# Kernel tuning notes

Hardware: AMD Instinct MI355X
Metric: run time of the kernel (lower is better)

## Reference

```python
import jax, jax.numpy as jnp
import numpy as np

B, NINP, NHID = 8192, 256, 1024
NB_IN, NB_OUT = 1, 8
BS_OUT = NHID // NB_OUT          # 128
ATT_OUT = BS_OUT * 4             # 512
TOPKVAL = 4


@jax.custom_vjp
def blocked_grad(x, mask):
    # forward is identity; backward masks the gradient (RIMs blocked_grad)
    return x

def _bg_fwd(x, mask):
    return x, mask

def _bg_bwd(mask, g):
    return (g * mask, jnp.zeros_like(mask))

blocked_grad.defvjp(_bg_fwd, _bg_bwd)


def setup_inputs() -> dict:
    key = jax.random.key(0)
    ks = jax.random.split(key, 12)
    p = lambda i, shape, s: s * jax.random.normal(ks[i], shape, dtype=jnp.float32)
    return {
        "inp": jax.random.normal(ks[0], (B, NB_IN * NINP), dtype=jnp.float32),
        "hx": jax.random.normal(ks[1], (B, NHID), dtype=jnp.float32),
        "step": 0,
        "Wq1": p(2, (NB_OUT, BS_OUT, 64), 0.01),
        "Wk1": p(3, (2, NINP, 64), 0.01),
        "Wv1": p(4, (2, NINP, ATT_OUT), 0.01),
        "Wq2": p(5, (NB_OUT, BS_OUT, 64), 0.01),
        "Wk2": p(6, (NB_OUT, BS_OUT, 64), 0.01),
        "Wv2": p(7, (NB_OUT, BS_OUT, 64), 0.01),
        "fc_w": p(8, (64, BS_OUT), 0.05),
        "fc_b": jnp.zeros((BS_OUT,), jnp.float32),
        "gate_w": p(9, (64, BS_OUT), 0.05),
        "gate_b": jnp.zeros((BS_OUT,), jnp.float32),
        "gru_wi": p(10, (NB_OUT, ATT_OUT, 3 * BS_OUT), 0.05),
        "gru_wh": p(11, (NB_OUT, BS_OUT, 3 * BS_OUT), 0.05),
        "gru_bi": jnp.zeros((NB_OUT, 3 * BS_OUT), jnp.float32),
        "gru_bh": jnp.zeros((NB_OUT, 3 * BS_OUT), jnp.float32),
    }


def _block_gru(x, h, wi, wh, bi, bh):
    # x: [B, K, ATT_OUT], h: [B, K, BS_OUT]; blockified GRUCell == per-block GRU
    gx = jnp.einsum('bkd,kde->bke', x, wi) + bi
    gh = jnp.einsum('bkd,kde->bke', h, wh) + bh
    xr, xz, xn = jnp.split(gx, 3, axis=-1)
    hr, hz, hn = jnp.split(gh, 3, axis=-1)
    r = jax.nn.sigmoid(xr + hr)
    z = jax.nn.sigmoid(xz + hz)
    n = jnp.tanh(xn + r * hn)
    return (1.0 - z) * n + z * h


def reference(inp, hx, step, Wq1, Wk1, Wv1, Wq2, Wk2, Wv2,
              fc_w, fc_b, gate_w, gate_b, gru_wi, gru_wh, gru_bi, gru_bh):
    b = inp.shape[0]
    x = inp.reshape(b, NB_IN, NINP)                              # repeat factor (num_modules_read_input-1)=1
    kv = jnp.concatenate([jnp.zeros_like(x[:, :1]), x], axis=1)  # [b, 2, NINP] (null slot first)
    hq = hx.reshape(b, NB_OUT, BS_OUT)

    # input attention (n_head=1, d_k=64, skip_write -> identity fc, no residual gating)
    q = jnp.einsum('bkd,kde->bke', hq, Wq1)                      # [b, 8, 64]
    kk = jnp.einsum('bmd,mde->bme', kv, Wk1)                     # [b, 2, 64]
    vv = jnp.einsum('bmd,mde->bme', kv, Wv1)                     # [b, 2, 512]
    iatt = jax.nn.softmax(jnp.einsum('bke,bme->bkm', q, kk) / 8.0, axis=-1)  # temp=sqrt(64)
    inp_use = jnp.einsum('bkm,bme->bke', iatt, vv)               # [b, 8, 512]

    # top-k block selection: zero out blocks most attentive to the null slot
    null_score = iatt[:, :, 0]
    _, bottom_idx = jax.lax.top_k(null_score, NB_OUT - TOPKVAL)
    mask = jnp.ones((b, NB_OUT), inp.dtype)
    mask = mask.at[jnp.arange(b)[:, None], bottom_idx].set(0.0)
    mask = jax.lax.stop_gradient(mask)

    hx_new = _block_gru(inp_use, hq, gru_wi, gru_wh, gru_bi, gru_bh)  # [b, 8, 128]

    # communication attention (n_head=4, d_k=d_v=16, gated residual form)
    g = blocked_grad(hx_new, mask[:, :, None])
    q2 = jnp.einsum('bkd,kde->bke', g, Wq2).reshape(b, NB_OUT, 4, 16)
    k2 = jnp.einsum('bkd,kde->bke', g, Wk2).reshape(b, NB_OUT, 4, 16)
    v2 = jnp.einsum('bkd,kde->bke', g, Wv2).reshape(b, NB_OUT, 4, 16)
    attn2 = jax.nn.softmax(jnp.einsum('bqhd,bkhd->bhqk', q2, k2) / 4.0, axis=-1)  # temp=sqrt(16)
    o = jnp.einsum('bhqk,bkhd->bqhd', attn2, v2).reshape(b, NB_OUT, 64)
    att = jax.nn.sigmoid(o @ gate_w + gate_b) * jnp.tanh(o @ fc_w + fc_b)  # [b, 8, 128]
    hx_new = hx_new + att

    mask_full = jnp.repeat(mask[:, :, None], BS_OUT, axis=2).reshape(b, NHID)
    hx_out = mask_full * hx_new.reshape(b, NHID) + (1.0 - mask_full) * hx
    return hx_out, mask_full
```

## Files before the change

kernel.cpp:

```cpp
#include <hip/hip_runtime.h>
#include <cstdint>
#include <cstddef>

#define NB 8192

typedef __attribute__((ext_vector_type(4))) float f32x4;
typedef __attribute__((ext_vector_type(8))) short bf16x8;

__device__ __forceinline__ float sigmoidf_(float x){ return 1.0f/(1.0f+expf(-x)); }

__device__ __forceinline__ unsigned short f2bf(float f){
    union { float f; unsigned u; } v; v.f = f;
    unsigned u = v.u;
    return (unsigned short)((u + 0x7fffu + ((u >> 16) & 1u)) >> 16);
}
__device__ __forceinline__ float bf2f(unsigned short b){
    union { unsigned u; float f; } v; v.u = ((unsigned)b) << 16;
    return v.f;
}
__device__ __forceinline__ void ld8f(const unsigned short* p, float* f){
    uint4 u = *(const uint4*)p;
    f[0]=bf2f(u.x&0xffff); f[1]=bf2f(u.x>>16);
    f[2]=bf2f(u.y&0xffff); f[3]=bf2f(u.y>>16);
    f[4]=bf2f(u.z&0xffff); f[5]=bf2f(u.z>>16);
    f[6]=bf2f(u.w&0xffff); f[7]=bf2f(u.w>>16);
}

__global__ __launch_bounds__(256) void gemm_nn(
    const float* __restrict__ A, int lda, int aZ,
    const float* __restrict__ W, int wZ, int ldw,
    float* __restrict__ C, int ldc, int cZ,
    int K)
{
    __shared__ float As[16][68];
    __shared__ float Ws[16][64];
    const int tid = threadIdx.x;
    const int tx = tid & 15, ty = tid >> 4;
    const int rowBase = blockIdx.y * 64;
    const int colBase = blockIdx.x * 64;
    A += (size_t)blockIdx.z * aZ;
    W += (size_t)blockIdx.z * wZ;
    C += (size_t)blockIdx.z * cZ;

    float acc[4][4] = {};
    for (int k0 = 0; k0 < K; k0 += 16) {
#pragma unroll
        for (int i = 0; i < 4; ++i) {
            int e = i * 256 + tid;
            int m = e >> 4, kk = e & 15;
            As[kk][m] = A[(size_t)(rowBase + m) * lda + (k0 + kk)];
        }
#pragma unroll
        for (int i = 0; i < 4; ++i) {
            int e = i * 256 + tid;
            int kk = e >> 6, n = e & 63;
            Ws[kk][n] = W[(size_t)(k0 + kk) * ldw + (colBase + n)];
        }
        __syncthreads();
#pragma unroll
        for (int kk = 0; kk < 16; ++kk) {
            const float4 a4 = *(const float4*)&As[kk][ty * 4];
            const float4 b4 = *(const float4*)&Ws[kk][tx * 4];
            const float a[4] = {a4.x, a4.y, a4.z, a4.w};
            const float b[4] = {b4.x, b4.y, b4.z, b4.w};
#pragma unroll
            for (int i = 0; i < 4; ++i)
#pragma unroll
                for (int j = 0; j < 4; ++j)
                    acc[i][j] = fmaf(a[i], b[j], acc[i][j]);
        }
        __syncthreads();
    }
#pragma unroll
    for (int i = 0; i < 4; ++i) {
        float* Cr = C + (size_t)(rowBase + ty * 4 + i) * ldc + colBase + tx * 4;
#pragma unroll
        for (int j = 0; j < 4; ++j) Cr[j] = acc[i][j];
    }
}

__global__ __launch_bounds__(256) void score_mask_k(
    const float* __restrict__ qbuf,
    const float* __restrict__ kk1,
    float* __restrict__ cbuf,
    float* __restrict__ maskb)
{
    const int b = blockIdx.x * 256 + threadIdx.x;
    const float* kr = kk1 + (size_t)b * 64;
    double s[8];
#pragma unroll
    for (int k = 0; k < 8; ++k) {
        const float* qr = qbuf + (size_t)b * 512 + k * 64;
        double acc = 0.0;
#pragma unroll
        for (int d = 0; d < 64; ++d) acc = fma((double)qr[d], (double)kr[d], acc);
        s[k] = acc / 8.0;
    }
#pragma unroll
    for (int k = 0; k < 8; ++k) {
        int rank = 0;
#pragma unroll
        for (int j = 0; j < 8; ++j)
            rank += (s[j] < s[k]) || (s[j] == s[k] && j < k);
        maskb[(size_t)b * 8 + k] = (rank < 4) ? 0.f : 1.f;
        cbuf[(size_t)b * 8 + k] = (float)(1.0 / (1.0 + exp(-s[k])));
    }
}

__global__ __launch_bounds__(256) void cast_bf(
    const float* __restrict__ inp, const float* __restrict__ hx,
    unsigned short* __restrict__ inp_bf, unsigned short* __restrict__ hx_bf)
{
    const int idx = blockIdx.x * 256 + threadIdx.x;
    const int NI = 524288;
    const float* src; unsigned short* dst; int i;
    if (idx < NI) { src = inp; dst = inp_bf; i = idx; }
    else          { src = hx;  dst = hx_bf;  i = idx - NI; }
    float4 v = *(const float4*)(src + (size_t)i * 4);
    uint2 u;
    u.x = (unsigned)f2bf(v.x) | ((unsigned)f2bf(v.y) << 16);
    u.y = (unsigned)f2bf(v.z) | ((unsigned)f2bf(v.w) << 16);
    *(uint2*)(dst + (size_t)i * 4) = u;
}

__global__ __launch_bounds__(256) void prep_w(
    const float* __restrict__ gwi, const float* __restrict__ gwh,
    const float* __restrict__ Wq2, const float* __restrict__ Wk2, const float* __restrict__ Wv2,
    const float* __restrict__ gate_w, const float* __restrict__ fc_w,
    unsigned short* __restrict__ wi_t,
    unsigned short* __restrict__ wh_t,
    unsigned short* __restrict__ w2_t,
    unsigned short* __restrict__ gfc_t)
{
    int idx = blockIdx.x * 256 + threadIdx.x;
    const int N1 = 8*384*512, N2 = 8*384*128, N3 = 8*192*128, N4 = 2*128*64;
    if (idx < N1) {
        int k = idx / 196608, r = idx % 196608, j = r / 512, e = r % 512;
        wi_t[idx] = f2bf(gwi[((size_t)k*512 + e)*384 + j]); return;
    }
    idx -= N1;
    if (idx < N2) {
        int k = idx / 49152, r = idx % 49152, j = r / 128, d = r % 128;
        wh_t[idx] = f2bf(gwh[((size_t)k*128 + d)*384 + j]); return;
    }
    idx -= N2;
    if (idx < N3) {
        int k = idx / 24576, r = idx % 24576, n = r / 128, d = r % 128;
        const float* Wsrc = (n < 64) ? Wq2 : ((n < 128) ? Wk2 : Wv2);
        w2_t[idx] = f2bf(Wsrc[((size_t)k*128 + d)*64 + (n & 63)]); return;
    }
    idx -= N3;
    if (idx < N4) {
        int g = idx / 8192, r = idx % 8192, j = r / 64, d = r % 64;
        gfc_t[idx] = f2bf((g ? fc_w : gate_w)[d*128 + j]);
    }
}

template<int ASRC_F32, int EPI>
__global__ __launch_bounds__(256) void gemm_bf(
    const void* __restrict__ Av, int lda, int aZ,
    const unsigned short* __restrict__ Bt, int bZ, int ldb,
    unsigned short* __restrict__ C, int ldc, long cZ,
    int K)
{
    __shared__ unsigned short As[64][72];
    __shared__ unsigned short Bs[64][72];
    const int tid = threadIdx.x;
    const int wave = tid >> 6, lane = tid & 63;
    const int wr = wave >> 1, wc = wave & 1;
    const int lr = lane & 15, lo = lane >> 4;
    const int rowBase = blockIdx.y * 64, colBase = blockIdx.x * 64;
    const int z = blockIdx.z;

    const f32x4 zero = {0.f, 0.f, 0.f, 0.f};
    f32x4 acc[2][2];
    acc[0][0]=zero; acc[0][1]=zero; acc[1][0]=zero; acc[1][1]=zero;

    const unsigned short* B = Bt + (size_t)z * bZ;
    for (int k0 = 0; k0 < K; k0 += 64) {
        if (ASRC_F32) {
            const float* A = (const float*)Av + (size_t)z * aZ;
#pragma unroll
            for (int i = 0; i < 4; ++i) {
                int c = i*256 + tid;
                int r = c >> 4, kc = (c & 15) << 2;
                float4 a4 = *(const float4*)(A + (size_t)(rowBase + r) * lda + k0 + kc);
                unsigned short* p = &As[r][kc];
                p[0]=f2bf(a4.x); p[1]=f2bf(a4.y); p[2]=f2bf(a4.z); p[3]=f2bf(a4.w);
            }
        } else {
            const unsigned short* A = (const unsigned short*)Av + (size_t)z * aZ;
#pragma unroll
            for (int i = 0; i < 2; ++i) {
                int c = i*256 + tid;
                int r = c >> 3, kc = (c & 7) << 3;
                *(uint4*)&As[r][kc] = *(const uint4*)(A + (size_t)(rowBase + r) * lda + k0 + kc);
            }
        }
#pragma unroll
        for (int i = 0; i < 2; ++i) {
            int c = i*256 + tid;
            int n = c >> 3, kc = (c & 7) << 3;
            *(uint4*)&Bs[n][kc] = *(const uint4*)(B + (size_t)(colBase + n) * ldb + k0 + kc);
        }
        __syncthreads();
#pragma unroll
        for (int ks = 0; ks < 64; ks += 32) {
            bf16x8 a0 = *(const bf16x8*)&As[wr*32 + lr][ks + lo*8];
            bf16x8 a1 = *(const bf16x8*)&As[wr*32 + 16 + lr][ks + lo*8];
            bf16x8 b0 = *(const bf16x8*)&Bs[wc*32 + lr][ks + lo*8];
            bf16x8 b1 = *(const bf16x8*)&Bs[wc*32 + 16 + lr][ks + lo*8];
            acc[0][0] = __builtin_amdgcn_mfma_f32_16x16x32_bf16(a0,b0,acc[0][0],0,0,0);
            acc[0][1] = __builtin_amdgcn_mfma_f32_16x16x32_bf16(a0,b1,acc[0][1],0,0,0);
            acc[1][0] = __builtin_amdgcn_mfma_f32_16x16x32_bf16(a1,b0,acc[1][0],0,0,0);
            acc[1][1] = __builtin_amdgcn_mfma_f32_16x16x32_bf16(a1,b1,acc[1][1],0,0,0);
        }
        __syncthreads();
    }
#pragma unroll
    for (int i = 0; i < 2; ++i)
#pragma unroll
    for (int j = 0; j < 2; ++j)
#pragma unroll
    for (int r = 0; r < 4; ++r) {
        int row = rowBase + wr*32 + i*16 + lo*4 + r;
        int col = colBase + wc*32 + j*16 + lr;
        float v = acc[i][j][r];
        if (EPI == 0) C[(size_t)row * ldc + (size_t)z * cZ + col] = f2bf(v);
        else          C[(size_t)z * cZ + (size_t)col * ldc + row] = f2bf(v);
    }
}

__global__ __launch_bounds__(256) void gemm_gxh(
    const unsigned short* __restrict__ inp_bf,
    const unsigned short* __restrict__ wc_t,
    const unsigned short* __restrict__ hx_bf,
    const unsigned short* __restrict__ wh_t,
    const float* __restrict__ cbuf,
    const float* __restrict__ gbi, const float* __restrict__ gbh,
    unsigned short* __restrict__ comb)
{
    __shared__ unsigned short As[64][72];
    __shared__ unsigned short Bs[128][72];
    const int tid = threadIdx.x;
    const int wave = tid >> 6, lane = tid & 63;
    const int wr = wave >> 1, wc = wave & 1;
    const int lr = lane & 15, lo = lane >> 4;
    const int rowBase = blockIdx.y * 64, colBase = blockIdx.x * 128;
    const int z = blockIdx.z;

    const f32x4 zero = {0.f, 0.f, 0.f, 0.f};
    f32x4 acc1[2][2][2], acc2[2][2][2];
#pragma unroll
    for (int t = 0; t < 2; ++t)
#pragma unroll
    for (int i = 0; i < 2; ++i)
#pragma unroll
    for (int j = 0; j < 2; ++j) { acc1[t][i][j] = zero; acc2[t][i][j] = zero; }

    const unsigned short* B1 = wc_t + (size_t)z * (384*256);
    for (int k0 = 0; k0 < 256; k0 += 64) {
#pragma unroll
        for (int i = 0; i < 2; ++i) {
            int c = i*256 + tid;
            int r = c >> 3, kc = (c & 7) << 3;
            *(uint4*)&As[r][kc] = *(const uint4*)(inp_bf + (size_t)(rowBase + r) * 256 + k0 + kc);
        }
#pragma unroll
        for (int i = 0; i < 4; ++i) {
            int c = i*256 + tid;
            int n = c >> 3, kc = (c & 7) << 3;
            *(uint4*)&Bs[n][kc] = *(const uint4*)(B1 + (size_t)(colBase + n) * 256 + k0 + kc);
        }
        __syncthreads();
#pragma unroll
        for (int ks = 0; ks < 64; ks += 32) {
            bf16x8 a0 = *(const bf16x8*)&As[wr*32 + lr][ks + lo*8];
            bf16x8 a1 = *(const bf16x8*)&As[wr*32 + 16 + lr][ks + lo*8];
#pragma unroll
            for (int t = 0; t < 2; ++t) {
                bf16x8 b0 = *(const bf16x8*)&Bs[t*64 + wc*32 + lr][ks + lo*8];
                bf16x8 b1 = *(const bf16x8*)&Bs[t*64 + wc*32 + 16 + lr][ks + lo*8];
                acc1[t][0][0] = __builtin_amdgcn_mfma_f32_16x16x32_bf16(a0,b0,acc1[t][0][0],0,0,0);
                acc1[t][0][1] = __builtin_amdgcn_mfma_f32_16x16x32_bf16(a0,b1,acc1[t][0][1],0,0,0);
                acc1[t][1][0] = __builtin_amdgcn_mfma_f32_16x16x32_bf16(a1,b0,acc1[t][1][0],0,0,0);
                acc1[t][1][1] = __builtin_amdgcn_mfma_f32_16x16x32_bf16(a1,b1,acc1[t][1][1],0,0,0);
            }
        }
        __syncthreads();
    }
    const unsigned short* B2 = wh_t + (size_t)z * (384*128);
    for (int k0 = 0; k0 < 128; k0 += 64) {
#pragma unroll
        for (int i = 0; i < 2; ++i) {
            int c = i*256 + tid;
            int r = c >> 3, kc = (c & 7) << 3;
            *(uint4*)&As[r][kc] = *(const uint4*)(hx_bf + (size_t)(rowBase + r) * 1024 + z*128 + k0 + kc);
        }
#pragma unroll
        for (int i = 0; i < 4; ++i) {
            int c = i*256 + tid;
            int n = c >> 3, kc = (c & 7) << 3;
            *(uint4*)&Bs[n][kc] = *(const uint4*)(B2 + (size_t)(colBase + n) * 128 + k0 + kc);
        }
        __syncthreads();
#pragma unroll
        for (int ks = 0; ks < 64; ks += 32) {
            bf16x8 a0 = *(const bf16x8*)&As[wr*32 + lr][ks + lo*8];
            bf16x8 a1 = *(const bf16x8*)&As[wr*32 + 16 + lr][ks + lo*8];
#pragma unroll
            for (int t = 0; t < 2; ++t) {
                bf16x8 b0 = *(const bf16x8*)&Bs[t*64 + wc*32 + lr][ks + lo*8];
                bf16x8 b1 = *(const bf16x8*)&Bs[t*64 + wc*32 + 16 + lr][ks + lo*8];
                acc2[t][0][0] = __builtin_amdgcn_mfma_f32_16x16x32_bf16(a0,b0,acc2[t][0][0],0,0,0);
                acc2[t][0][1] = __builtin_amdgcn_mfma_f32_16x16x32_bf16(a0,b1,acc2[t][0][1],0,0,0);
                acc2[t][1][0] = __builtin_amdgcn_mfma_f32_16x16x32_bf16(a1,b0,acc2[t][1][0],0,0,0);
                acc2[t][1][1] = __builtin_amdgcn_mfma_f32_16x16x32_bf16(a1,b1,acc2[t][1][1],0,0,0);
            }
        }
        __syncthreads();
    }
#pragma unroll
    for (int t = 0; t < 2; ++t)
#pragma unroll
    for (int i = 0; i < 2; ++i)
#pragma unroll
    for (int j = 0; j < 2; ++j)
#pragma unroll
    for (int r = 0; r < 4; ++r) {
        int row = rowBase + wr*32 + i*16 + lo*4 + r;
        int col = colBase + t*64 + wc*32 + j*16 + lr;
        float c = cbuf[(size_t)row * 8 + z];
        float v1 = fmaf(c, acc1[t][i][j][r], gbi[z*384 + col]);
        float v2 = acc2[t][i][j][r] + gbh[z*384 + col];
        size_t base = ((size_t)z * 8192 + row) * 512;
        if (col < 256) comb[base + col] = f2bf(v1 + v2);
        else { comb[base + col] = f2bf(v1); comb[base + col + 128] = f2bf(v2); }
    }
}

__global__ __launch_bounds__(256) void gru_all(
    const unsigned short* __restrict__ comb, const float* __restrict__ hx,
    unsigned short* __restrict__ hxn)
{
    const int idx = blockIdx.x * 256 + threadIdx.x;
    const int j = idx & 127, k = (idx >> 7) & 7, b = idx >> 10;
    const size_t base = ((size_t)k * 8192 + b) * 512;
    const float rz = bf2f(comb[base + j]);
    const float zz = bf2f(comb[base + 128 + j]);
    const float xn = bf2f(comb[base + 256 + j]);
    const float hn = bf2f(comb[base + 384 + j]);
    const float r = sigmoidf_(rz), z = sigmoidf_(zz);
    const float n = tanhf(fmaf(r, hn, xn));
    const float h = hx[idx];
    hxn[idx] = f2bf((1.f - z) * n + z * h);
}

__global__ __launch_bounds__(256) void attn2_bf(
    const unsigned short* __restrict__ qkv, unsigned short* __restrict__ o)
{
    const int idx = blockIdx.x * 256 + threadIdx.x;
    const int qb = idx & 7, h = (idx >> 3) & 3, b = idx >> 5;
    const unsigned short* rowb = qkv + (size_t)b * 1536;
    float qv[16];
    ld8f(rowb + qb*192 + h*16, qv); ld8f(rowb + qb*192 + h*16 + 8, qv + 8);
    float sc[8]; float mx = -1e30f;
#pragma unroll
    for (int kb = 0; kb < 8; ++kb) {
        float kv[16];
        ld8f(rowb + kb*192 + 64 + h*16, kv); ld8f(rowb + kb*192 + 64 + h*16 + 8, kv + 8);
        float a = 0.f;
#pragma unroll
        for (int d = 0; d < 16; ++d) a = fmaf(qv[d], kv[d], a);
        sc[kb] = a * 0.25f;
        mx = fmaxf(mx, sc[kb]);
    }
    float sum = 0.f;
#pragma unroll
    for (int kb = 0; kb < 8; ++kb) { sc[kb] = expf(sc[kb] - mx); sum += sc[kb]; }
    const float inv = 1.f / sum;
    float oa[16];
#pragma unroll
    for (int d = 0; d < 16; ++d) oa[d] = 0.f;
#pragma unroll
    for (int kb = 0; kb < 8; ++kb) {
        float vv[16];
        ld8f(rowb + kb*192 + 128 + h*16, vv); ld8f(rowb + kb*192 + 128 + h*16 + 8, vv + 8);
#pragma unroll
        for (int d = 0; d < 16; ++d) oa[d] = fmaf(sc[kb], vv[d], oa[d]);
    }
    unsigned short t[16];
#pragma unroll
    for (int d = 0; d < 16; ++d) t[d] = f2bf(oa[d] * inv);
    uint4 u0, u1;
    u0.x = (unsigned)t[0] | ((unsigned)t[1]<<16);  u0.y = (unsigned)t[2] | ((unsigned)t[3]<<16);
    u0.z = (unsigned)t[4] | ((unsigned)t[5]<<16);  u0.w = (unsigned)t[6] | ((unsigned)t[7]<<16);
    u1.x = (unsigned)t[8] | ((unsigned)t[9]<<16);  u1.y = (unsigned)t[10]| ((unsigned)t[11]<<16);
    u1.z = (unsigned)t[12]| ((unsigned)t[13]<<16); u1.w = (unsigned)t[14]| ((unsigned)t[15]<<16);
    unsigned short* op = o + (size_t)(b*8 + qb) * 64 + h*16;
    *(uint4*)op = u0; *(uint4*)(op + 8) = u1;
}

__global__ __launch_bounds__(256) void gatefc_final(
    const unsigned short* __restrict__ o,
    const unsigned short* __restrict__ gfc_t,
    const float* __restrict__ gate_b, const float* __restrict__ fc_b,
    const unsigned short* __restrict__ hxn,
    const float* __restrict__ hx,
    const float* __restrict__ maskb,
    float* __restrict__ out)
{
    __shared__ unsigned short As[64][72];
    __shared__ unsigned short Bg[64][72];
    __shared__ unsigned short Bf[64][72];
    const int tid = threadIdx.x;
    const int wave = tid >> 6, lane = tid & 63;
    const int wr = wave >> 1, wc = wave & 1;
    const int lr = lane & 15, lo = lane >> 4;
    const int rowBase = blockIdx.y * 64, colBase = blockIdx.x * 64;

#pragma unroll
    for (int i = 0; i < 2; ++i) {
        int c = i*256 + tid;
        int r = c >> 3, kc = (c & 7) << 3;
        *(uint4*)&As[r][kc] = *(const uint4*)(o + (size_t)(rowBase + r) * 64 + kc);
        *(uint4*)&Bg[r][kc] = *(const uint4*)(gfc_t + (size_t)(colBase + r) * 64 + kc);
        *(uint4*)&Bf[r][kc] = *(const uint4*)(gfc_t + 8192 + (size_t)(colBase + r) * 64 + kc);
    }
    __syncthreads();

    const f32x4 zero = {0.f, 0.f, 0.f, 0.f};
    f32x4 ag[2][2], af[2][2];
    ag[0][0]=zero; ag[0][1]=zero; ag[1][0]=zero; ag[1][1]=zero;
    af[0][0]=zero; af[0][1]=zero; af[1][0]=zero; af[1][1]=zero;
#pragma unroll
    for (int ks = 0; ks < 64; ks += 32) {
        bf16x8 a0 = *(const bf16x8*)&As[wr*32 + lr][ks + lo*8];
        bf16x8 a1 = *(const bf16x8*)&As[wr*32 + 16 + lr][ks + lo*8];
        bf16x8 g0 = *(const bf16x8*)&Bg[wc*32 + lr][ks + lo*8];
        bf16x8 g1 = *(const bf16x8*)&Bg[wc*32 + 16 + lr][ks + lo*8];
        bf16x8 f0 = *(const bf16x8*)&Bf[wc*32 + lr][ks + lo*8];
        bf16x8 f1 = *(const bf16x8*)&Bf[wc*32 + 16 + lr][ks + lo*8];
        ag[0][0] = __builtin_amdgcn_mfma_f32_16x16x32_bf16(a0,g0,ag[0][0],0,0,0);
        ag[0][1] = __builtin_amdgcn_mfma_f32_16x16x32_bf16(a0,g1,ag[0][1],0,0,0);
        ag[1][0] = __builtin_amdgcn_mfma_f32_16x16x32_bf16(a1,g0,ag[1][0],0,0,0);
        ag[1][1] = __builtin_amdgcn_mfma_f32_16x16x32_bf16(a1,g1,ag[1][1],0,0,0);
        af[0][0] = __builtin_amdgcn_mfma_f32_16x16x32_bf16(a0,f0,af[0][0],0,0,0);
        af[0][1] = __builtin_amdgcn_mfma_f32_16x16x32_bf16(a0,f1,af[0][1],0,0,0);
        af[1][0] = __builtin_amdgcn_mfma_f32_16x16x32_bf16(a1,f0,af[1][0],0,0,0);
        af[1][1] = __builtin_amdgcn_mfma_f32_16x16x32_bf16(a1,f1,af[1][1],0,0,0);
    }
#pragma unroll
    for (int i = 0; i < 2; ++i)
#pragma unroll
    for (int j = 0; j < 2; ++j)
#pragma unroll
    for (int r = 0; r < 4; ++r) {
        int m   = rowBase + wr*32 + i*16 + lo*4 + r;
        int col = colBase + wc*32 + j*16 + lr;
        float g = sigmoidf_(ag[i][j][r] + gate_b[col]);
        float f = tanhf(af[i][j][r] + fc_b[col]);
        float att = g * f;
        size_t oidx = (size_t)m * 128 + col;
        float msk = maskb[m];
        float hnv = bf2f(hxn[oidx]) + att;
        out[oidx] = msk * hnv + (1.f - msk) * hx[oidx];
        out[(size_t)NB * 1024 + oidx] = msk;
    }
}

extern "C" void kernel_launch(void* const* d_in, const int* in_sizes, int n_in,
                              void* d_out, int out_size, void* d_ws, size_t ws_size,
                              hipStream_t stream)
{
    (void)in_sizes; (void)n_in; (void)out_size; (void)ws_size;
    const float* inp    = (const float*)d_in[0];
    const float* hx     = (const float*)d_in[1];
    const float* Wq1    = (const float*)d_in[3];
    const float* Wk1    = (const float*)d_in[4];
    const float* Wv1    = (const float*)d_in[5];
    const float* Wq2    = (const float*)d_in[6];
    const float* Wk2    = (const float*)d_in[7];
    const float* Wv2    = (const float*)d_in[8];
    const float* fc_w   = (const float*)d_in[9];
    const float* fc_b   = (const float*)d_in[10];
    const float* gate_w = (const float*)d_in[11];
    const float* gate_b = (const float*)d_in[12];
    const float* gwi    = (const float*)d_in[13];
    const float* gwh    = (const float*)d_in[14];
    const float* gbi    = (const float*)d_in[15];
    const float* gbh    = (const float*)d_in[16];
    float* out = (float*)d_out;

    char* W = (char*)d_ws;
    float* cbuf  = (float*)(W + 0x0);
    float* maskb = (float*)(W + 0x40000);
    float* kk1f  = (float*)(W + 0x80000);
    float* qbuff = (float*)(W + 0x280000);
    unsigned short* inp_bf = (unsigned short*)(W + 0x1280000);
    unsigned short* hx_bf  = (unsigned short*)(W + 0x1680000);
    unsigned short* wi_t   = (unsigned short*)(W + 0x2680000);
    unsigned short* wh_t   = (unsigned short*)(W + 0x2980000);
    unsigned short* w2_t   = (unsigned short*)(W + 0x2A40000);
    unsigned short* gfc_t  = (unsigned short*)(W + 0x2AA0000);
    unsigned short* wc_t   = (unsigned short*)(W + 0x2AA8000);
    unsigned short* comb   = (unsigned short*)(W + 0x2C28000);
    unsigned short* hxn    = (unsigned short*)(W + 0x6C28000);
    unsigned short* qkv    = comb;
    unsigned short* o_bf   = (unsigned short*)(W + 0x2C28000 + 25165824);

    const dim3 blk(256);

    gemm_nn<<<dim3(1, 128, 1), blk, 0, stream>>>(inp, 256, 0, Wk1 + 256*64, 0, 64, kk1f, 64, 0, 256);
    gemm_nn<<<dim3(1, 128, 8), blk, 0, stream>>>(hx, 1024, 128, Wq1, 128*64, 64, qbuff, 512, 64, 128);
    score_mask_k<<<dim3(32), blk, 0, stream>>>(qbuff, kk1f, cbuf, maskb);

    cast_bf<<<dim3(10240), blk, 0, stream>>>(inp, hx, inp_bf, hx_bf);
    prep_w<<<dim3(8512), blk, 0, stream>>>(gwi, gwh, Wq2, Wk2, Wv2, gate_w, fc_w,
                                           wi_t, wh_t, w2_t, gfc_t);

    gemm_bf<1, 1><<<dim3(6, 4, 8), blk, 0, stream>>>(
        Wv1 + 256*512, 512, 0, wi_t, 384*512, 512, wc_t, 256, (long)384*256, 512);

    gemm_gxh<<<dim3(3, 128, 8), blk, 0, stream>>>(inp_bf, wc_t, hx_bf, wh_t, cbuf, gbi, gbh, comb);

    gru_all<<<dim3(32768), blk, 0, stream>>>(comb, hx, hxn);

    gemm_bf<0, 0><<<dim3(3, 128, 8), blk, 0, stream>>>(
        hxn, 1024, 128, w2_t, 192*128, 128, qkv, 1536, 192L, 128);

    attn2_bf<<<dim3(1024), blk, 0, stream>>>(qkv, o_bf);

    gatefc_final<<<dim3(2, 1024), blk, 0, stream>>>(o_bf, gfc_t, gate_b, fc_b,
                                                    hxn, hx, maskb, out);
}
```

Baseline: 372.8 us.

## Fuse GRU gate epilogue into gate GEMM and move score GEMMs to split-bf16 MFMA

The GRU elementwise pass is folded into the gate GEMM epilogue. Weight columns are repacked so each block holds matching r/z/n column groups, which removes the large intermediate comb buffer and its separate kernel. The fp32 FMA score GEMMs become a single MFMA kernel that uses hi/lo bf16 splitting (four MFMAs per tile) to keep near-fp32 accuracy for the top-k mask. The cast and weight-prep kernels are merged into one, and the Wv1×gwi combine reads the fp32 weights directly. The cost is more MFMA work and register pressure in the fused kernel, plus a small risk that the split-bf16 scores flip mask decisions relative to fp64.

```diff
diff --git a/kernel.cpp b/kernel.cpp
--- a/kernel.cpp
+++ b/kernel.cpp
@@ -25,65 +25,152 @@
     f[4]=bf2f(u.z&0xffff); f[5]=bf2f(u.z>>16);
     f[6]=bf2f(u.w&0xffff); f[7]=bf2f(u.w>>16);
 }
-
-__global__ __launch_bounds__(256) void gemm_nn(
-    const float* __restrict__ A, int lda, int aZ,
-    const float* __restrict__ W, int wZ, int ldw,
-    float* __restrict__ C, int ldc, int cZ,
-    int K)
-{
-    __shared__ float As[16][68];
-    __shared__ float Ws[16][64];
+#define MFMA16(a,b,c) __builtin_amdgcn_mfma_f32_16x16x32_bf16(a,b,c,0,0,0)
+
+__global__ __launch_bounds__(256) void prep_all(
+    const float* __restrict__ inp, const float* __restrict__ hx,
+    const float* __restrict__ gwh,
+    const float* __restrict__ Wq2, const float* __restrict__ Wk2, const float* __restrict__ Wv2,
+    const float* __restrict__ gate_w, const float* __restrict__ fc_w,
+    const float* __restrict__ Wq1, const float* __restrict__ Wk1,
+    unsigned short* __restrict__ inp_bf, unsigned short* __restrict__ hx_bf,
+    unsigned short* __restrict__ whp,
+    unsigned short* __restrict__ w2_t,
+    unsigned short* __restrict__ gfc_t,
+    unsigned short* __restrict__ wq1t_hi, unsigned short* __restrict__ wq1t_lo,
+    unsigned short* __restrict__ wk1t_hi, unsigned short* __restrict__ wk1t_lo)
+{
+    int idx = blockIdx.x * 256 + threadIdx.x;
+    if (idx < 524288) {
+        float4 v = *(const float4*)(inp + (size_t)idx * 4);
+        uint2 u;
+        u.x = (unsigned)f2bf(v.x) | ((unsigned)f2bf(v.y) << 16);
+        u.y = (unsigned)f2bf(v.z) | ((unsigned)f2bf(v.w) << 16);
+        *(uint2*)(inp_bf + (size_t)idx * 4) = u; return;
+    }
+    idx -= 524288;
+    if (idx < 2097152) {
+        float4 v = *(const float4*)(hx + (size_t)idx * 4);
+        uint2 u;
+        u.x = (unsigned)f2bf(v.x) | ((unsigned)f2bf(v.y) << 16);
+        u.y = (unsigned)f2bf(v.z) | ((unsigned)f2bf(v.w) << 16);
+        *(uint2*)(hx_bf + (size_t)idx * 4) = u; return;
+    }
+    idx -= 2097152;
+    if (idx < 393216) {
+        int k = idx / 49152, rem = idx % 49152, cp = rem / 128, d = rem % 128;
+        int b2 = cp / 192, r2 = cp % 192, g = r2 / 64, jjl = r2 % 64;
+        int j = g * 128 + b2 * 64 + jjl;
+        whp[idx] = f2bf(gwh[((size_t)k * 128 + d) * 384 + j]); return;
+    }
+    idx -= 393216;
+    if (idx < 196608) {
+        int k = idx / 24576, r = idx % 24576, n = r / 128, d = r % 128;
+        const float* Wsrc = (n < 64) ? Wq2 : ((n < 128) ? Wk2 : Wv2);
+        w2_t[idx] = f2bf(Wsrc[((size_t)k * 128 + d) * 64 + (n & 63)]); return;
+    }
+    idx -= 196608;
+    if (idx < 16384) {
+        int g = idx / 8192, r = idx % 8192, j = r / 64, d = r % 64;
+        gfc_t[idx] = f2bf((g ? fc_w : gate_w)[d * 128 + j]); return;
+    }
+    idx -= 16384;
+    if (idx < 65536) {
+        int k = idx / 8192, rem = idx % 8192, e = rem / 128, d = rem % 128;
+        float s = Wq1[((size_t)k * 128 + d) * 64 + e];
+        unsigned short h = f2bf(s);
+        wq1t_hi[idx] = h; wq1t_lo[idx] = f2bf(s - bf2f(h)); return;
+    }
+    idx -= 65536;
+    if (idx < 16384) {
+        int e = idx / 256, d = idx % 256;
+        float s = Wk1[16384 + d * 64 + e];
+        unsigned short h = f2bf(s);
+        wk1t_hi[idx] = h; wk1t_lo[idx] = f2bf(s - bf2f(h));
+    }
+}
+
+__global__ __launch_bounds__(256) void gemm_score(
+    const float* __restrict__ inp, const float* __restrict__ hx,
+    const unsigned short* __restrict__ wq1t_hi, const unsigned short* __restrict__ wq1t_lo,
+    const unsigned short* __restrict__ wk1t_hi, const unsigned short* __restrict__ wk1t_lo,
+    float* __restrict__ qbuff, float* __restrict__ kk1f)
+{
+    __shared__ unsigned short AsH[64][72], AsL[64][72], BsH[64][72], BsL[64][72];
     const int tid = threadIdx.x;
-    const int tx = tid & 15, ty = tid >> 4;
+    const int wave = tid >> 6, lane = tid & 63;
+    const int wr = wave >> 1, wc = wave & 1;
+    const int lr = lane & 15, lo = lane >> 4;
     const int rowBase = blockIdx.y * 64;
-    const int colBase = blockIdx.x * 64;
-    A += (size_t)blockIdx.z * aZ;
-    W += (size_t)blockIdx.z * wZ;
-    C += (size_t)blockIdx.z * cZ;
-
-    float acc[4][4] = {};
-    for (int k0 = 0; k0 < K; k0 += 16) {
+    const int z = blockIdx.z;
+    const int K   = (z == 8) ? 256 : 128;
+    const float* A = (z == 8) ? inp : hx;
+    const int lda  = (z == 8) ? 256 : 1024;
+    const int coff = (z == 8) ? 0 : z * 128;
+    const unsigned short* Bh = (z == 8) ? wk1t_hi : wq1t_hi + z * 8192;
+    const unsigned short* Bl = (z == 8) ? wk1t_lo : wq1t_lo + z * 8192;
+    const int ldb = K;
+
+    const f32x4 zero = {0.f,0.f,0.f,0.f};
+    f32x4 acc[2][2]; acc[0][0]=zero; acc[0][1]=zero; acc[1][0]=zero; acc[1][1]=zero;
+
+    for (int k0 = 0; k0 < K; k0 += 64) {
 #pragma unroll
         for (int i = 0; i < 4; ++i) {
-            int e = i * 256 + tid;
-            int m = e >> 4, kk = e & 15;
-            As[kk][m] = A[(size_t)(rowBase + m) * lda + (k0 + kk)];
-        }
-#pragma unroll
-        for (int i = 0; i < 4; ++i) {
-            int e = i * 256 + tid;
-            int kk = e >> 6, n = e & 63;
-            Ws[kk][n] = W[(size_t)(k0 + kk) * ldw + (colBase + n)];
-        }
-        __syncthreads();
-#pragma unroll
-        for (int kk = 0; kk < 16; ++kk) {
-            const float4 a4 = *(const float4*)&As[kk][ty * 4];
-            const float4 b4 = *(const float4*)&Ws[kk][tx * 4];
-            const float a[4] = {a4.x, a4.y, a4.z, a4.w};
-            const float b[4] = {b4.x, b4.y, b4.z, b4.w};
-#pragma unroll
-            for (int i = 0; i < 4; ++i)
-#pragma unroll
-                for (int j = 0; j < 4; ++j)
-                    acc[i][j] = fmaf(a[i], b[j], acc[i][j]);
-        }
-        __syncthreads();
-    }
-#pragma unroll
-    for (int i = 0; i < 4; ++i) {
-        float* Cr = C + (size_t)(rowBase + ty * 4 + i) * ldc + colBase + tx * 4;
-#pragma unroll
-        for (int j = 0; j < 4; ++j) Cr[j] = acc[i][j];
+            int c = i*256 + tid; int r = c >> 4, kc = (c & 15) << 2;
+            float4 v = *(const float4*)(A + (size_t)(rowBase + r) * lda + coff + k0 + kc);
+            unsigned short h0=f2bf(v.x), h1=f2bf(v.y), h2=f2bf(v.z), h3=f2bf(v.w);
+            AsH[r][kc]=h0; AsH[r][kc+1]=h1; AsH[r][kc+2]=h2; AsH[r][kc+3]=h3;
+            AsL[r][kc]  =f2bf(v.x - bf2f(h0)); AsL[r][kc+1]=f2bf(v.y - bf2f(h1));
+            AsL[r][kc+2]=f2bf(v.z - bf2f(h2)); AsL[r][kc+3]=f2bf(v.w - bf2f(h3));
+        }
+#pragma unroll
+        for (int i = 0; i < 2; ++i) {
+            int c = i*256 + tid; int n = c >> 3, kc = (c & 7) << 3;
+            *(uint4*)&BsH[n][kc] = *(const uint4*)(Bh + (size_t)n * ldb + k0 + kc);
+            *(uint4*)&BsL[n][kc] = *(const uint4*)(Bl + (size_t)n * ldb + k0 + kc);
+        }
+        __syncthreads();
+#pragma unroll
+        for (int ks = 0; ks < 64; ks += 32) {
+            bf16x8 aH[2], aL[2], bH[2], bL[2];
+            aH[0] = *(const bf16x8*)&AsH[wr*32 + lr][ks + lo*8];
+            aH[1] = *(const bf16x8*)&AsH[wr*32 + 16 + lr][ks + lo*8];
+            aL[0] = *(const bf16x8*)&AsL[wr*32 + lr][ks + lo*8];
+            aL[1] = *(const bf16x8*)&AsL[wr*32 + 16 + lr][ks + lo*8];
+            bH[0] = *(const bf16x8*)&BsH[wc*32 + lr][ks + lo*8];
+            bH[1] = *(const bf16x8*)&BsH[wc*32 + 16 + lr][ks + lo*8];
+            bL[0] = *(const bf16x8*)&BsL[wc*32 + lr][ks + lo*8];
+            bL[1] = *(const bf16x8*)&BsL[wc*32 + 16 + lr][ks + lo*8];
+#pragma unroll
+            for (int i = 0; i < 2; ++i)
+#pragma unroll
+            for (int j = 0; j < 2; ++j) {
+                acc[i][j] = MFMA16(aH[i], bH[j], acc[i][j]);
+                acc[i][j] = MFMA16(aH[i], bL[j], acc[i][j]);
+                acc[i][j] = MFMA16(aL[i], bH[j], acc[i][j]);
+                acc[i][j] = MFMA16(aL[i], bL[j], acc[i][j]);
+            }
+        }
+        __syncthreads();
+    }
+#pragma unroll
+    for (int i = 0; i < 2; ++i)
+#pragma unroll
+    for (int jf = 0; jf < 2; ++jf)
+#pragma unroll
+    for (int r4 = 0; r4 < 4; ++r4) {
+        int row = rowBase + wr*32 + i*16 + lo*4 + r4;
+        int col = wc*32 + jf*16 + lr;
+        float v = acc[i][jf][r4];
+        if (z == 8) kk1f[(size_t)row * 64 + col] = v;
+        else        qbuff[(size_t)row * 512 + z * 64 + col] = v;
     }
 }
 
 __global__ __launch_bounds__(256) void score_mask_k(
-    const float* __restrict__ qbuf,
-    const float* __restrict__ kk1,
-    float* __restrict__ cbuf,
-    float* __restrict__ maskb)
+    const float* __restrict__ qbuf, const float* __restrict__ kk1,
+    float* __restrict__ cbuf, float* __restrict__ maskb)
 {
     const int b = blockIdx.x * 256 + threadIdx.x;
     const float* kr = kk1 + (size_t)b * 64;
@@ -107,61 +194,9 @@
     }
 }
 
-__global__ __launch_bounds__(256) void cast_bf(
-    const float* __restrict__ inp, const float* __restrict__ hx,
-    unsigned short* __restrict__ inp_bf, unsigned short* __restrict__ hx_bf)
-{
-    const int idx = blockIdx.x * 256 + threadIdx.x;
-    const int NI = 524288;
-    const float* src; unsigned short* dst; int i;
-    if (idx < NI) { src = inp; dst = inp_bf; i = idx; }
-    else          { src = hx;  dst = hx_bf;  i = idx - NI; }
-    float4 v = *(const float4*)(src + (size_t)i * 4);
-    uint2 u;
-    u.x = (unsigned)f2bf(v.x) | ((unsigned)f2bf(v.y) << 16);
-    u.y = (unsigned)f2bf(v.z) | ((unsigned)f2bf(v.w) << 16);
-    *(uint2*)(dst + (size_t)i * 4) = u;
-}
-
-__global__ __launch_bounds__(256) void prep_w(
-    const float* __restrict__ gwi, const float* __restrict__ gwh,
-    const float* __restrict__ Wq2, const float* __restrict__ Wk2, const float* __restrict__ Wv2,
-    const float* __restrict__ gate_w, const float* __restrict__ fc_w,
-    unsigned short* __restrict__ wi_t,
-    unsigned short* __restrict__ wh_t,
-    unsigned short* __restrict__ w2_t,
-    unsigned short* __restrict__ gfc_t)
-{
-    int idx = blockIdx.x * 256 + threadIdx.x;
-    const int N1 = 8*384*512, N2 = 8*384*128, N3 = 8*192*128, N4 = 2*128*64;
-    if (idx < N1) {
-        int k = idx / 196608, r = idx % 196608, j = r / 512, e = r % 512;
-        wi_t[idx] = f2bf(gwi[((size_t)k*512 + e)*384 + j]); return;
-    }
-    idx -= N1;
-    if (idx < N2) {
-        int k = idx / 49152, r = idx % 49152, j = r / 128, d = r % 128;
-        wh_t[idx] = f2bf(gwh[((size_t)k*128 + d)*384 + j]); return;
-    }
-    idx -= N2;
-    if (idx < N3) {
-        int k = idx / 24576, r = idx % 24576, n = r / 128, d = r % 128;
-        const float* Wsrc = (n < 64) ? Wq2 : ((n < 128) ? Wk2 : Wv2);
-        w2_t[idx] = f2bf(Wsrc[((size_t)k*128 + d)*64 + (n & 63)]); return;
-    }
-    idx -= N3;
-    if (idx < N4) {
-        int g = idx / 8192, r = idx % 8192, j = r / 64, d = r % 64;
-        gfc_t[idx] = f2bf((g ? fc_w : gate_w)[d*128 + j]);
-    }
-}
-
-template<int ASRC_F32, int EPI>
-__global__ __launch_bounds__(256) void gemm_bf(
-    const void* __restrict__ Av, int lda, int aZ,
-    const unsigned short* __restrict__ Bt, int bZ, int ldb,
-    unsigned short* __restrict__ C, int ldc, long cZ,
-    int K)
+__global__ __launch_bounds__(256) void gemm_wcomb(
+    const float* __restrict__ Wv1, const float* __restrict__ gwi,
+    unsigned short* __restrict__ wcp)
 {
     __shared__ unsigned short As[64][72];
     __shared__ unsigned short Bs[64][72];
@@ -171,37 +206,26 @@
     const int lr = lane & 15, lo = lane >> 4;
     const int rowBase = blockIdx.y * 64, colBase = blockIdx.x * 64;
     const int z = blockIdx.z;
-
-    const f32x4 zero = {0.f, 0.f, 0.f, 0.f};
-    f32x4 acc[2][2];
-    acc[0][0]=zero; acc[0][1]=zero; acc[1][0]=zero; acc[1][1]=zero;
-
-    const unsigned short* B = Bt + (size_t)z * bZ;
-    for (int k0 = 0; k0 < K; k0 += 64) {
-        if (ASRC_F32) {
-            const float* A = (const float*)Av + (size_t)z * aZ;
-#pragma unroll
-            for (int i = 0; i < 4; ++i) {
-                int c = i*256 + tid;
-                int r = c >> 4, kc = (c & 15) << 2;
-                float4 a4 = *(const float4*)(A + (size_t)(rowBase + r) * lda + k0 + kc);
-                unsigned short* p = &As[r][kc];
-                p[0]=f2bf(a4.x); p[1]=f2bf(a4.y); p[2]=f2bf(a4.z); p[3]=f2bf(a4.w);
-            }
-        } else {
-            const unsigned short* A = (const unsigned short*)Av + (size_t)z * aZ;
-#pragma unroll
-            for (int i = 0; i < 2; ++i) {
-                int c = i*256 + tid;
-                int r = c >> 3, kc = (c & 7) << 3;
-                *(uint4*)&As[r][kc] = *(const uint4*)(A + (size_t)(rowBase + r) * lda + k0 + kc);
-            }
-        }
-#pragma unroll
-        for (int i = 0; i < 2; ++i) {
-            int c = i*256 + tid;
-            int n = c >> 3, kc = (c & 7) << 3;
-            *(uint4*)&Bs[n][kc] = *(const uint4*)(B + (size_t)(colBase + n) * ldb + k0 + kc);
+    const float* A = Wv1 + 131072;
+    const float* B = gwi + (size_t)z * 196608;
+
+    const f32x4 zero = {0.f,0.f,0.f,0.f};
+    f32x4 acc[2][2]; acc[0][0]=zero; acc[0][1]=zero; acc[1][0]=zero; acc[1][1]=zero;
+
+    for (int k0 = 0; k0 < 512; k0 += 64) {
+#pragma unroll
+        for (int i = 0; i < 4; ++i) {
+            int c = i*256 + tid; int r = c >> 4, kc = (c & 15) << 2;
+            float4 v = *(const float4*)(A + (size_t)(rowBase + r) * 512 + k0 + kc);
+            unsigned short* p = &As[r][kc];
+            p[0]=f2bf(v.x); p[1]=f2bf(v.y); p[2]=f2bf(v.z); p[3]=f2bf(v.w);
+        }
+#pragma unroll
+        for (int i = 0; i < 4; ++i) {
+            int c = i*256 + tid; int kk = c >> 4, nc = (c & 15) << 2;
+            float4 v = *(const float4*)(B + (size_t)(k0 + kk) * 384 + colBase + nc);
+            Bs[nc+0][kk]=f2bf(v.x); Bs[nc+1][kk]=f2bf(v.y);
+            Bs[nc+2][kk]=f2bf(v.z); Bs[nc+3][kk]=f2bf(v.w);
         }
         __syncthreads();
 #pragma unroll
@@ -210,150 +234,221 @@
             bf16x8 a1 = *(const bf16x8*)&As[wr*32 + 16 + lr][ks + lo*8];
             bf16x8 b0 = *(const bf16x8*)&Bs[wc*32 + lr][ks + lo*8];
             bf16x8 b1 = *(const bf16x8*)&Bs[wc*32 + 16 + lr][ks + lo*8];
-            acc[0][0] = __builtin_amdgcn_mfma_f32_16x16x32_bf16(a0,b0,acc[0][0],0,0,0);
-            acc[0][1] = __builtin_amdgcn_mfma_f32_16x16x32_bf16(a0,b1,acc[0][1],0,0,0);
-            acc[1][0] = __builtin_amdgcn_mfma_f32_16x16x32_bf16(a1,b0,acc[1][0],0,0,0);
-            acc[1][1] = __builtin_amdgcn_mfma_f32_16x16x32_bf16(a1,b1,acc[1][1],0,0,0);
-        }
-        __syncthreads();
-    }
-#pragma unroll
-    for (int i = 0; i < 2; ++i)
-#pragma unroll
-    for (int j = 0; j < 2; ++j)
-#pragma unroll
-    for (int r = 0; r < 4; ++r) {
-        int row = rowBase + wr*32 + i*16 + lo*4 + r;
-        int col = colBase + wc*32 + j*16 + lr;
-        float v = acc[i][j][r];
-        if (EPI == 0) C[(size_t)row * ldc + (size_t)z * cZ + col] = f2bf(v);
-        else          C[(size_t)z * cZ + (size_t)col * ldc + row] = f2bf(v);
-    }
-}
-
-__global__ __launch_bounds__(256) void gemm_gxh(
+            acc[0][0] = MFMA16(a0,b0,acc[0][0]); acc[0][1] = MFMA16(a0,b1,acc[0][1]);
+            acc[1][0] = MFMA16(a1,b0,acc[1][0]); acc[1][1] = MFMA16(a1,b1,acc[1][1]);
+        }
+        __syncthreads();
+    }
+#pragma unroll
+    for (int i = 0; i < 2; ++i)
+#pragma unroll
+    for (int jf = 0; jf < 2; ++jf)
+#pragma unroll
+    for (int r4 = 0; r4 < 4; ++r4) {
+        int row = rowBase + wr*32 + i*16 + lo*4 + r4;
+        int n = colBase + wc*32 + jf*16 + lr;
+        int g = n >> 7, jjf = n & 127;
+        int c2 = (jjf >> 6) * 192 + g * 64 + (jjf & 63);
+        wcp[(size_t)z*98304 + (size_t)c2*256 + row] = f2bf(acc[i][jf][r4]);
+    }
+}
+
+__global__ __launch_bounds__(256) void gemm_gxh_fused(
     const unsigned short* __restrict__ inp_bf,
-    const unsigned short* __restrict__ wc_t,
+    const unsigned short* __restrict__ wcp,
     const unsigned short* __restrict__ hx_bf,
-    const unsigned short* __restrict__ wh_t,
+    const unsigned short* __restrict__ whp,
     const float* __restrict__ cbuf,
     const float* __restrict__ gbi, const float* __restrict__ gbh,
-    unsigned short* __restrict__ comb)
+    const float* __restrict__ hx,
+    unsigned short* __restrict__ hxn)
 {
     __shared__ unsigned short As[64][72];
-    __shared__ unsigned short Bs[128][72];
+    __shared__ unsigned short Bs[192][72];
     const int tid = threadIdx.x;
     const int wave = tid >> 6, lane = tid & 63;
     const int wr = wave >> 1, wc = wave & 1;
     const int lr = lane & 15, lo = lane >> 4;
-    const int rowBase = blockIdx.y * 64, colBase = blockIdx.x * 128;
+    const int b2 = blockIdx.x, j0 = b2 * 64;
+    const int rowBase = blockIdx.y * 64;
     const int z = blockIdx.z;
 
-    const f32x4 zero = {0.f, 0.f, 0.f, 0.f};
-    f32x4 acc1[2][2][2], acc2[2][2][2];
-#pragma unroll
-    for (int t = 0; t < 2; ++t)
-#pragma unroll
-    for (int i = 0; i < 2; ++i)
-#pragma unroll
-    for (int j = 0; j < 2; ++j) { acc1[t][i][j] = zero; acc2[t][i][j] = zero; }
-
-    const unsigned short* B1 = wc_t + (size_t)z * (384*256);
-    for (int k0 = 0; k0 < 256; k0 += 64) {
+    const f32x4 zero = {0.f,0.f,0.f,0.f};
+    f32x4 arz[2][2][2], anx[2][2], anh[2][2];
+#pragma unroll
+    for (int g = 0; g < 2; ++g)
+#pragma unroll
+    for (int i = 0; i < 2; ++i)
+#pragma unroll
+    for (int j = 0; j < 2; ++j) arz[g][i][j] = zero;
+#pragma unroll
+    for (int i = 0; i < 2; ++i)
+#pragma unroll
+    for (int j = 0; j < 2; ++j) { anx[i][j] = zero; anh[i][j] = zero; }
+
+    uint4 ra[2], rb[6];
+    auto LOADT = [&](int t) {
 #pragma unroll
         for (int i = 0; i < 2; ++i) {
-            int c = i*256 + tid;
-            int r = c >> 3, kc = (c & 7) << 3;
-            *(uint4*)&As[r][kc] = *(const uint4*)(inp_bf + (size_t)(rowBase + r) * 256 + k0 + kc);
-        }
-#pragma unroll
-        for (int i = 0; i < 4; ++i) {
-            int c = i*256 + tid;
-            int n = c >> 3, kc = (c & 7) << 3;
-            *(uint4*)&Bs[n][kc] = *(const uint4*)(B1 + (size_t)(colBase + n) * 256 + k0 + kc);
-        }
-        __syncthreads();
+            int c = i*256 + tid; int r = c >> 3, kc = (c & 7) << 3;
+            const unsigned short* src = (t < 4)
+                ? inp_bf + (size_t)(rowBase + r) * 256 + t*64 + kc
+                : hx_bf + (size_t)(rowBase + r) * 1024 + z*128 + (t-4)*64 + kc;
+            ra[i] = *(const uint4*)src;
+        }
+#pragma unroll
+        for (int i = 0; i < 6; ++i) {
+            int c = i*256 + tid; int n = c >> 3, kc = (c & 7) << 3;
+            const unsigned short* src = (t < 4)
+                ? wcp + (size_t)z*98304 + (size_t)(b2*192 + n) * 256 + t*64 + kc
+                : whp + (size_t)z*49152 + (size_t)(b2*192 + n) * 128 + (t-4)*64 + kc;
+            rb[i] = *(const uint4*)src;
+        }
+    };
+    LOADT(0);
+#pragma unroll
+    for (int t = 0; t < 6; ++t) {
+        __syncthreads();
+#pragma unroll
+        for (int i = 0; i < 2; ++i) { int c = i*256 + tid; *(uint4*)&As[c>>3][(c&7)<<3] = ra[i]; }
+#pragma unroll
+        for (int i = 0; i < 6; ++i) { int c = i*256 + tid; *(uint4*)&Bs[c>>3][(c&7)<<3] = rb[i]; }
+        __syncthreads();
+        if (t < 5) LOADT(t + 1);
 #pragma unroll
         for (int ks = 0; ks < 64; ks += 32) {
             bf16x8 a0 = *(const bf16x8*)&As[wr*32 + lr][ks + lo*8];
             bf16x8 a1 = *(const bf16x8*)&As[wr*32 + 16 + lr][ks + lo*8];
 #pragma unroll
-            for (int t = 0; t < 2; ++t) {
-                bf16x8 b0 = *(const bf16x8*)&Bs[t*64 + wc*32 + lr][ks + lo*8];
-                bf16x8 b1 = *(const bf16x8*)&Bs[t*64 + wc*32 + 16 + lr][ks + lo*8];
-                acc1[t][0][0] = __builtin_amdgcn_mfma_f32_16x16x32_bf16(a0,b0,acc1[t][0][0],0,0,0);
-                acc1[t][0][1] = __builtin_amdgcn_mfma_f32_16x16x32_bf16(a0,b1,acc1[t][0][1],0,0,0);
-                acc1[t][1][0] = __builtin_amdgcn_mfma_f32_16x16x32_bf16(a1,b0,acc1[t][1][0],0,0,0);
-                acc1[t][1][1] = __builtin_amdgcn_mfma_f32_16x16x32_bf16(a1,b1,acc1[t][1][1],0,0,0);
+            for (int g = 0; g < 3; ++g) {
+                bf16x8 b0 = *(const bf16x8*)&Bs[g*64 + wc*32 + lr][ks + lo*8];
+                bf16x8 b1 = *(const bf16x8*)&Bs[g*64 + wc*32 + 16 + lr][ks + lo*8];
+                if (g < 2) {
+                    arz[g][0][0] = MFMA16(a0,b0,arz[g][0][0]);
+                    arz[g][0][1] = MFMA16(a0,b1,arz[g][0][1]);
+                    arz[g][1][0] = MFMA16(a1,b0,arz[g][1][0]);
+                    arz[g][1][1] = MFMA16(a1,b1,arz[g][1][1]);
+                } else if (t < 4) {
+                    anx[0][0] = MFMA16(a0,b0,anx[0][0]);
+                    anx[0][1] = MFMA16(a0,b1,anx[0][1]);
+                    anx[1][0] = MFMA16(a1,b0,anx[1][0]);
+                    anx[1][1] = MFMA16(a1,b1,anx[1][1]);
+                } else {
+                    anh[0][0] = MFMA16(a0,b0,anh[0][0]);
+                    anh[0][1] = MFMA16(a0,b1,anh[0][1]);
+                    anh[1][0] = MFMA16(a1,b0,anh[1][0]);
+                    anh[1][1] = MFMA16(a1,b1,anh[1][1]);
+                }
             }
         }
-        __syncthreads();
-    }
-    const unsigned short* B2 = wh_t + (size_t)z * (384*128);
-    for (int k0 = 0; k0 < 128; k0 += 64) {
+        if (t == 3) {
+#pragma unroll
+            for (int i = 0; i < 2; ++i)
+#pragma unroll
+            for (int r4 = 0; r4 < 4; ++r4) {
+                int row = rowBase + wr*32 + i*16 + lo*4 + r4;
+                float cc = cbuf[(size_t)row * 8 + z];
+                arz[0][i][0][r4] *= cc; arz[0][i][1][r4] *= cc;
+                arz[1][i][0][r4] *= cc; arz[1][i][1][r4] *= cc;
+                anx[i][0][r4] *= cc;    anx[i][1][r4] *= cc;
+            }
+        }
+    }
+    const float* bi = gbi + z * 384;
+    const float* bh = gbh + z * 384;
+#pragma unroll
+    for (int i = 0; i < 2; ++i)
+#pragma unroll
+    for (int jf = 0; jf < 2; ++jf)
+#pragma unroll
+    for (int r4 = 0; r4 < 4; ++r4) {
+        int row = rowBase + wr*32 + i*16 + lo*4 + r4;
+        int jj = wc*32 + jf*16 + lr;
+        int j = j0 + jj;
+        float xr = arz[0][i][jf][r4] + bi[j]       + bh[j];
+        float xz = arz[1][i][jf][r4] + bi[128 + j] + bh[128 + j];
+        float xn = anx[i][jf][r4]    + bi[256 + j];
+        float hn = anh[i][jf][r4]    + bh[256 + j];
+        float r = sigmoidf_(xr), zz = sigmoidf_(xz);
+        float n = tanhf(fmaf(r, hn, xn));
+        float h = hx[(size_t)row * 1024 + z*128 + j];
+        hxn[(size_t)row * 1024 + z*128 + j] = f2bf((1.f - zz) * n + zz * h);
+    }
+}
+
+__global__ __launch_bounds__(256) void gemm_qkv(
+    const unsigned short* __restrict__ hxn,
+    const unsigned short* __restrict__ w2_t,
+    unsigned short* __restrict__ qkv)
+{
+    __shared__ unsigned short As[64][72];
+    __shared__ unsigned short Bs[192][72];
+    const int tid = threadIdx.x;
+    const int wave = tid >> 6, lane = tid & 63;
+    const int wr = wave >> 1, wc = wave & 1;
+    const int lr = lane & 15, lo = lane >> 4;
+    const int rowBase = blockIdx.y * 64;
+    const int z = blockIdx.z;
+
+    const f32x4 zero = {0.f,0.f,0.f,0.f};
+    f32x4 acc[3][2][2];
+#pragma unroll
+    for (int g = 0; g < 3; ++g)
+#pragma unroll
+    for (int i = 0; i < 2; ++i)
+#pragma unroll
+    for (int j = 0; j < 2; ++j) acc[g][i][j] = zero;
+
+    uint4 ra[2], rb[6];
+    auto LOADT = [&](int t) {
 #pragma unroll
         for (int i = 0; i < 2; ++i) {
-            int c = i*256 + tid;
-            int r = c >> 3, kc = (c & 7) << 3;
-            *(uint4*)&As[r][kc] = *(const uint4*)(hx_bf + (size_t)(rowBase + r) * 1024 + z*128 + k0 + kc);
-        }
-#pragma unroll
-        for (int i = 0; i < 4; ++i) {
-            int c = i*256 + tid;
-            int n = c >> 3, kc = (c & 7) << 3;
-            *(uint4*)&Bs[n][kc] = *(const uint4*)(B2 + (size_t)(colBase + n) * 128 + k0 + kc);
-        }
-        __syncthreads();
+            int c = i*256 + tid; int r = c >> 3, kc = (c & 7) << 3;
+            ra[i] = *(const uint4*)(hxn + (size_t)(rowBase + r) * 1024 + z*128 + t*64 + kc);
+        }
+#pragma unroll
+        for (int i = 0; i < 6; ++i) {
+            int c = i*256 + tid; int n = c >> 3, kc = (c & 7) << 3;
+            rb[i] = *(const uint4*)(w2_t + (size_t)z*24576 + (size_t)n * 128 + t*64 + kc);
+        }
+    };
+    LOADT(0);
+#pragma unroll
+    for (int t = 0; t < 2; ++t) {
+        __syncthreads();
+#pragma unroll
+        for (int i = 0; i < 2; ++i) { int c = i*256 + tid; *(uint4*)&As[c>>3][(c&7)<<3] = ra[i]; }
+#pragma unroll
+        for (int i = 0; i < 6; ++i) { int c = i*256 + tid; *(uint4*)&Bs[c>>3][(c&7)<<3] = rb[i]; }
+        __syncthreads();
+        if (t < 1) LOADT(t + 1);
 #pragma unroll
         for (int ks = 0; ks < 64; ks += 32) {
             bf16x8 a0 = *(const bf16x8*)&As[wr*32 + lr][ks + lo*8];
             bf16x8 a1 = *(const bf16x8*)&As[wr*32 + 16 + lr][ks + lo*8];
 #pragma unroll
-            for (int t = 0; t < 2; ++t) {
-                bf16x8 b0 = *(const bf16x8*)&Bs[t*64 + wc*32 + lr][ks + lo*8];
-                bf16x8 b1 = *(const bf16x8*)&Bs[t*64 + wc*32 + 16 + lr][ks + lo*8];
-                acc2[t][0][0] = __builtin_amdgcn_mfma_f32_16x16x32_bf16(a0,b0,acc2[t][0][0],0,0,0);
-                acc2[t][0][1] = __builtin_amdgcn_mfma_f32_16x16x32_bf16(a0,b1,acc2[t][0][1],0,0,0);
-                acc2[t][1][0] = __builtin_amdgcn_mfma_f32_16x16x32_bf16(a1,b0,acc2[t][1][0],0,0,0);
-                acc2[t][1][1] = __builtin_amdgcn_mfma_f32_16x16x32_bf16(a1,b1,acc2[t][1][1],0,0,0);
+            for (int g = 0; g < 3; ++g) {
+                bf16x8 b0 = *(const bf16x8*)&Bs[g*64 + wc*32 + lr][ks + lo*8];
+                bf16x8 b1 = *(const bf16x8*)&Bs[g*64 + wc*32 + 16 + lr][ks + lo*8];
+                acc[g][0][0] = MFMA16(a0,b0,acc[g][0][0]);
+                acc[g][0][1] = MFMA16(a0,b1,acc[g][0][1]);
+                acc[g][1][0] = MFMA16(a1,b0,acc[g][1][0]);
+                acc[g][1][1] = MFMA16(a1,b1,acc[g][1][1]);
             }
         }
-        __syncthreads();
-    }
-#pragma unroll
-    for (int t = 0; t < 2; ++t)
-#pragma unroll
-    for (int i = 0; i < 2; ++i)
-#pragma unroll
-    for (int j = 0; j < 2; ++j)
-#pragma unroll
-    for (int r = 0; r < 4; ++r) {
-        int row = rowBase + wr*32 + i*16 + lo*4 + r;
-        int col = colBase + t*64 + wc*32 + j*16 + lr;
-        float c = cbuf[(size_t)row * 8 + z];
-        float v1 = fmaf(c, acc1[t][i][j][r], gbi[z*384 + col]);
-        float v2 = acc2[t][i][j][r] + gbh[z*384 + col];
-        size_t base = ((size_t)z * 8192 + row) * 512;
-        if (col < 256) comb[base + col] = f2bf(v1 + v2);
-        else { comb[base + col] = f2bf(v1); comb[base + col + 128] = f2bf(v2); }
-    }
-}
-
-__global__ __launch_bounds__(256) void gru_all(
-    const unsigned short* __restrict__ comb, const float* __restrict__ hx,
-    unsigned short* __restrict__ hxn)
-{
-    const int idx = blockIdx.x * 256 + threadIdx.x;
-    const int j = idx & 127, k = (idx >> 7) & 7, b = idx >> 10;
-    const size_t base = ((size_t)k * 8192 + b) * 512;
-    const float rz = bf2f(comb[base + j]);
-    const float zz = bf2f(comb[base + 128 + j]);
-    const float xn = bf2f(comb[base + 256 + j]);
-    const float hn = bf2f(comb[base + 384 + j]);
-    const float r = sigmoidf_(rz), z = sigmoidf_(zz);
-    const float n = tanhf(fmaf(r, hn, xn));
-    const float h = hx[idx];
-    hxn[idx] = f2bf((1.f - z) * n + z * h);
+    }
+#pragma unroll
+    for (int g = 0; g < 3; ++g)
+#pragma unroll
+    for (int i = 0; i < 2; ++i)
+#pragma unroll
+    for (int jf = 0; jf < 2; ++jf)
+#pragma unroll
+    for (int r4 = 0; r4 < 4; ++r4) {
+        int row = rowBase + wr*32 + i*16 + lo*4 + r4;
+        int c = g*64 + wc*32 + jf*16 + lr;
+        qkv[(size_t)row * 1536 + z*192 + c] = f2bf(acc[g][i][jf][r4]);
+    }
 }
 
 __global__ __launch_bounds__(256) void attn2_bf(
@@ -429,7 +524,7 @@
     }
     __syncthreads();
 
-    const f32x4 zero = {0.f, 0.f, 0.f, 0.f};
+    const f32x4 zero = {0.f,0.f,0.f,0.f};
     f32x4 ag[2][2], af[2][2];
     ag[0][0]=zero; ag[0][1]=zero; ag[1][0]=zero; ag[1][1]=zero;
     af[0][0]=zero; af[0][1]=zero; af[1][0]=zero; af[1][1]=zero;
@@ -441,25 +536,21 @@
         bf16x8 g1 = *(const bf16x8*)&Bg[wc*32 + 16 + lr][ks + lo*8];
         bf16x8 f0 = *(const bf16x8*)&Bf[wc*32 + lr][ks + lo*8];
         bf16x8 f1 = *(const bf16x8*)&Bf[wc*32 + 16 + lr][ks + lo*8];
-        ag[0][0] = __builtin_amdgcn_mfma_f32_16x16x32_bf16(a0,g0,ag[0][0],0,0,0);
-        ag[0][1] = __builtin_amdgcn_mfma_f32_16x16x32_bf16(a0,g1,ag[0][1],0,0,0);
-        ag[1][0] = __builtin_amdgcn_mfma_f32_16x16x32_bf16(a1,g0,ag[1][0],0,0,0);
-        ag[1][1] = __builtin_amdgcn_mfma_f32_16x16x32_bf16(a1,g1,ag[1][1],0,0,0);
-        af[0][0] = __builtin_amdgcn_mfma_f32_16x16x32_bf16(a0,f0,af[0][0],0,0,0);
-        af[0][1] = __builtin_amdgcn_mfma_f32_16x16x32_bf16(a0,f1,af[0][1],0,0,0);
-        af[1][0] = __builtin_amdgcn_mfma_f32_16x16x32_bf16(a1,f0,af[1][0],0,0,0);
-        af[1][1] = __builtin_amdgcn_mfma_f32_16x16x32_bf16(a1,f1,af[1][1],0,0,0);
-    }
-#pragma unroll
-    for (int i = 0; i < 2; ++i)
-#pragma unroll
-    for (int j = 0; j < 2; ++j)
-#pragma unroll
-    for (int r = 0; r < 4; ++r) {
-        int m   = rowBase + wr*32 + i*16 + lo*4 + r;
-        int col = colBase + wc*32 + j*16 + lr;
-        float g = sigmoidf_(ag[i][j][r] + gate_b[col]);
-        float f = tanhf(af[i][j][r] + fc_b[col]);
+        ag[0][0] = MFMA16(a0,g0,ag[0][0]); ag[0][1] = MFMA16(a0,g1,ag[0][1]);
+        ag[1][0] = MFMA16(a1,g0,ag[1][0]); ag[1][1] = MFMA16(a1,g1,ag[1][1]);
+        af[0][0] = MFMA16(a0,f0,af[0][0]); af[0][1] = MFMA16(a0,f1,af[0][1]);
+        af[1][0] = MFMA16(a1,f0,af[1][0]); af[1][1] = MFMA16(a1,f1,af[1][1]);
+    }
+#pragma unroll
+    for (int i = 0; i < 2; ++i)
+#pragma unroll
+    for (int jf = 0; jf < 2; ++jf)
+#pragma unroll
+    for (int r4 = 0; r4 < 4; ++r4) {
+        int m   = rowBase + wr*32 + i*16 + lo*4 + r4;
+        int col = colBase + wc*32 + jf*16 + lr;
+        float g = sigmoidf_(ag[i][jf][r4] + gate_b[col]);
+        float f = tanhf(af[i][jf][r4] + fc_b[col]);
         float att = g * f;
         size_t oidx = (size_t)m * 128 + col;
         float msk = maskb[m];
@@ -497,40 +588,33 @@
     float* maskb = (float*)(W + 0x40000);
     float* kk1f  = (float*)(W + 0x80000);
     float* qbuff = (float*)(W + 0x280000);
-    unsigned short* inp_bf = (unsigned short*)(W + 0x1280000);
-    unsigned short* hx_bf  = (unsigned short*)(W + 0x1680000);
-    unsigned short* wi_t   = (unsigned short*)(W + 0x2680000);
-    unsigned short* wh_t   = (unsigned short*)(W + 0x2980000);
-    unsigned short* w2_t   = (unsigned short*)(W + 0x2A40000);
-    unsigned short* gfc_t  = (unsigned short*)(W + 0x2AA0000);
-    unsigned short* wc_t   = (unsigned short*)(W + 0x2AA8000);
-    unsigned short* comb   = (unsigned short*)(W + 0x2C28000);
-    unsigned short* hxn    = (unsigned short*)(W + 0x6C28000);
-    unsigned short* qkv    = comb;
-    unsigned short* o_bf   = (unsigned short*)(W + 0x2C28000 + 25165824);
+    unsigned short* inp_bf   = (unsigned short*)(W + 0x1280000);
+    unsigned short* hx_bf    = (unsigned short*)(W + 0x1680000);
+    unsigned short* whp      = (unsigned short*)(W + 0x2680000);
+    unsigned short* w2_t     = (unsigned short*)(W + 0x2740000);
+    unsigned short* gfc_t    = (unsigned short*)(W + 0x27A0000);
+    unsigned short* wq1t_hi  = (unsigned short*)(W + 0x27A8000);
+    unsigned short* wq1t_lo  = (unsigned short*)(W + 0x27C8000);
+    unsigned short* wk1t_hi  = (unsigned short*)(W + 0x27E8000);
+    unsigned short* wk1t_lo  = (unsigned short*)(W + 0x27F0000);
+    unsigned short* wcp      = (unsigned short*)(W + 0x27F8000);
+    unsigned short* hxn      = (unsigned short*)(W + 0x2978000);
+    unsigned short* qkv      = (unsigned short*)(W + 0x3978000);
+    unsigned short* o_bf     = (unsigned short*)(W + 0x5178000);
 
     const dim3 blk(256);
 
-    gemm_nn<<<dim3(1, 128, 1), blk, 0, stream>>>(inp, 256, 0, Wk1 + 256*64, 0, 64, kk1f, 64, 0, 256);
-    gemm_nn<<<dim3(1, 128, 8), blk, 0, stream>>>(hx, 1024, 128, Wq1, 128*64, 64, qbuff, 512, 64, 128);
+    gemm_wcomb<<<dim3(6, 4, 8), blk, 0, stream>>>(Wv1, gwi, wcp);
+    prep_all<<<dim3(12928), blk, 0, stream>>>(inp, hx, gwh, Wq2, Wk2, Wv2, gate_w, fc_w,
+                                              Wq1, Wk1, inp_bf, hx_bf, whp, w2_t, gfc_t,
+                                              wq1t_hi, wq1t_lo, wk1t_hi, wk1t_lo);
+    gemm_score<<<dim3(1, 128, 9), blk, 0, stream>>>(inp, hx, wq1t_hi, wq1t_lo,
+                                                    wk1t_hi, wk1t_lo, qbuff, kk1f);
     score_mask_k<<<dim3(32), blk, 0, stream>>>(qbuff, kk1f, cbuf, maskb);
-
-    cast_bf<<<dim3(10240), blk, 0, stream>>>(inp, hx, inp_bf, hx_bf);
-    prep_w<<<dim3(8512), blk, 0, stream>>>(gwi, gwh, Wq2, Wk2, Wv2, gate_w, fc_w,
-                                           wi_t, wh_t, w2_t, gfc_t);
-
-    gemm_bf<1, 1><<<dim3(6, 4, 8), blk, 0, stream>>>(
-        Wv1 + 256*512, 512, 0, wi_t, 384*512, 512, wc_t, 256, (long)384*256, 512);
-
-    gemm_gxh<<<dim3(3, 128, 8), blk, 0, stream>>>(inp_bf, wc_t, hx_bf, wh_t, cbuf, gbi, gbh, comb);
-
-    gru_all<<<dim3(32768), blk, 0, stream>>>(comb, hx, hxn);
-
-    gemm_bf<0, 0><<<dim3(3, 128, 8), blk, 0, stream>>>(
-        hxn, 1024, 128, w2_t, 192*128, 128, qkv, 1536, 192L, 128);
-
+    gemm_gxh_fused<<<dim3(2, 128, 8), blk, 0, stream>>>(inp_bf, wcp, hx_bf, whp,
+                                                        cbuf, gbi, gbh, hx, hxn);
+    gemm_qkv<<<dim3(1, 128, 8), blk, 0, stream>>>(hxn, w2_t, qkv);
     attn2_bf<<<dim3(1024), blk, 0, stream>>>(qkv, o_bf);
-
     gatefc_final<<<dim3(2, 1024), blk, 0, stream>>>(o_bf, gfc_t, gate_b, fc_b,
                                                     hxn, hx, maskb, out);
 }
```

Result: slower. 416.1 us (+11.6%).
